# Kernel optimization log

Hardware: AMD Instinct MI355X
Metric: run time of the kernel (lower is better)

The kernel has to match this reference:

```python
import jax, jax.numpy as jnp
import numpy as np

N, D, F, H, L = 500000, 2, 128, 128, 8
OMEGA_0 = 30.0


def setup_inputs() -> dict:
    key = jax.random.key(0)
    ks = jax.random.split(key, 13)
    two_pi = 2.0 * np.pi
    w = 0.05  # weight init scale
    return {
        "S": jax.random.uniform(ks[0], (N, 1), jnp.float32),
        "t": jax.random.uniform(ks[1], (N, 1), jnp.float32),
        "B": jax.random.normal(ks[2], (D, F), jnp.float32) * two_pi,
        "in_w": jax.random.normal(ks[3], (2 * F, H), jnp.float32) * w,
        "in_b": jax.random.normal(ks[4], (H,), jnp.float32) * w,
        "blk_w1": jax.random.normal(ks[5], (L, H, H), jnp.float32) * w,
        "blk_b1": jax.random.normal(ks[6], (L, H), jnp.float32) * w,
        "blk_w2": jax.random.normal(ks[7], (L, H, H), jnp.float32) * w,
        "blk_b2": jax.random.normal(ks[8], (L, H), jnp.float32) * w,
        "skip_w": jax.random.normal(ks[9], ((L + 1) // 2, 2 * F, H), jnp.float32) * w,
        "skip_b": jax.random.normal(ks[10], ((L + 1) // 2, H), jnp.float32) * w,
        "out_w": jax.random.normal(ks[11], (H, 1), jnp.float32) * w,
        "out_b": jax.random.normal(ks[12], (1,), jnp.float32) * w,
    }


def reference(S, t, B, in_w, in_b, blk_w1, blk_b1, blk_w2, blk_b2,
              skip_w, skip_b, out_w, out_b):
    # Fourier feature mapping: [N,2] -> [N,2F]
    inputs = jnp.concatenate([S, t], axis=1)
    proj = inputs @ B                       # [N, F]
    ff = jnp.concatenate([jnp.sin(proj), jnp.cos(proj)], axis=-1)  # [N, 2F]
    # SIREN input layer
    x = jnp.sin(OMEGA_0 * (ff @ in_w + in_b))  # [N, H]
    n_blocks = blk_w1.shape[0]
    for i in range(n_blocks):  # small fixed layer loop
        h = jnp.tanh(x @ blk_w1[i] + blk_b1[i]) @ blk_w2[i] + blk_b2[i]
        x = x + h  # residual
        if i % 2 == 0:  # periodic skip from Fourier features
            x = x + ff @ skip_w[i // 2] + skip_b[i // 2]
    return x @ out_w + out_b  # [N, 1]
```

## Files before the change

kernel.cpp:

```cpp
#include <hip/hip_runtime.h>
#include <cstdint>
#include <cstddef>

#define NPTS 500000

using f16   = _Float16;
using f16x8 = __attribute__((ext_vector_type(8))) _Float16;
using f32x4 = __attribute__((ext_vector_type(4))) float;
using f32x16= __attribute__((ext_vector_type(16))) float;

#define WS_INW   0u
#define WS_SKIP  65536u
#define WS_W1    327680u
#define WS_W2    589824u
#define WS_BIAS  851968u
#define WS_BC    863232u
#define WS_OB    864256u
#define WS_TOTAL 864272u

__device__ __host__ __forceinline__ int phi(int m) {
  return (m & ~12) | ((m & 4) << 1) | ((m & 8) >> 1);
}

extern "C" __global__ void pinn_prep(const float* __restrict__ in_w,
                                     const float* __restrict__ w1,
                                     const float* __restrict__ w2,
                                     const float* __restrict__ skw,
                                     const float* __restrict__ inb,
                                     const float* __restrict__ b1,
                                     const float* __restrict__ b2,
                                     const float* __restrict__ skb,
                                     const float* __restrict__ ow,
                                     const float* __restrict__ ob,
                                     const float* __restrict__ Bg,
                                     char* __restrict__ ws) {
  int idx = (int)blockIdx.x * 256 + (int)threadIdx.x;
  if (idx < 32768) {
    int H = idx >> 14, r = idx & 16383, m = r >> 7, c = r & 127;
    int gl = c >> 5, sc = (c >> 4) & 1, lo = c & 15;
    int k = sc * 128 + (H * 4 + gl) * 16 + lo;
    uint32_t off = (uint32_t)(m * 256 + c * 2) ^ (uint32_t)((m & 15) << 4);
    *(f16*)(ws + WS_INW + (uint32_t)H * 32768u + off) = (f16)in_w[k * 128 + phi(m)];
  } else if (idx < 163840) {
    int r0 = idx - 32768;
    int j4 = r0 >> 15, rr = r0 & 32767;
    int H = rr >> 14, r = rr & 16383, m = r >> 7, c = r & 127;
    int gl = c >> 5, sc = (c >> 4) & 1, lo = c & 15;
    int k = sc * 128 + (H * 4 + gl) * 16 + lo;
    uint32_t off = (uint32_t)(m * 256 + c * 2) ^ (uint32_t)((m & 15) << 4);
    *(f16*)(ws + WS_SKIP + (uint32_t)j4 * 65536u + (uint32_t)H * 32768u + off) =
        (f16)skw[(j4 * 256 + k) * 128 + phi(m)];
  } else if (idx < 294912) {
    int r0 = idx - 163840;
    int i = r0 >> 14, r = r0 & 16383, m = r >> 7, k = r & 127;
    uint32_t off = (uint32_t)(m * 256 + k * 2) ^ (uint32_t)((m & 15) << 4);
    *(f16*)(ws + WS_W1 + (uint32_t)i * 32768u + off) = (f16)w1[(i * 128 + k) * 128 + phi(m)];
  } else if (idx < 425984) {
    int r0 = idx - 294912;
    int i = r0 >> 14, r = r0 & 16383, m = r >> 7, k = r & 127;
    uint32_t off = (uint32_t)(m * 256 + k * 2) ^ (uint32_t)((m & 15) << 4);
    *(f16*)(ws + WS_W2 + (uint32_t)i * 32768u + off) = (f16)w2[(i * 128 + k) * 128 + phi(m)];
  } else if (idx < 428800) {
    int r = idx - 425984;
    int M = r >> 7, pos = r & 127;
    int pp = phi(pos);
    float v;
    if (M == 0)        v = inb[pp];
    else if (M <= 16)  { int t = M - 1; int i = t >> 1; v = (t & 1) ? b2[i * 128 + pp] : b1[i * 128 + pp]; }
    else if (M <= 20)  v = skb[(M - 17) * 128 + pp];
    else               v = ow[pp];
    *(float*)(ws + WS_BIAS + (uint32_t)r * 4u) = v;
  } else if (idx < 429056) {
    int r = idx - 428800;
    int slot = r >> 4, e2 = r & 15;
    int kq = slot >> 1, hb = slot & 1;
    int row = e2 >> 3, e = e2 & 7;
    int j = kq * 16 + hb * 8 + e;
    *(float*)(ws + WS_BC + (uint32_t)r * 4u) = Bg[row * 128 + j] * 0.15915494309189535f;
  } else if (idx == 429056) {
    *(float*)(ws + WS_OB) = ob[0];
    *(float*)(ws + WS_OB + 4) = 0.f; *(float*)(ws + WS_OB + 8) = 0.f; *(float*)(ws + WS_OB + 12) = 0.f;
  }
}

__device__ __forceinline__ float ftanh(float x) {
  float e = __builtin_amdgcn_exp2f(x * 2.8853901817f);
  return 1.0f - 2.0f * __builtin_amdgcn_rcpf(e + 1.0f);
}
__device__ __forceinline__ float fsin_rev(float rev) {
  return __builtin_amdgcn_sinf(__builtin_amdgcn_fractf(rev));
}

__device__ __forceinline__ void gll16(const char* g, char* l) {
  __builtin_amdgcn_global_load_lds((const __attribute__((address_space(1))) void*)g,
                                   (__attribute__((address_space(3))) void*)l, 16, 0, 0);
}
__device__ __forceinline__ void stage32(const char* g, char* l, int wv, int ln64) {
  const char* gs = g + wv * 4096 + ln64 * 16;
  char* ls = l + wv * 4096;
  #pragma unroll
  for (int it = 0; it < 4; ++it) gll16(gs + it * 1024, ls + it * 1024);
}

#define MFMA_(a,b,c)  __builtin_amdgcn_mfma_f32_32x32x16_f16(a,b,c,0,0,0)

#define LDW(BASE, MT, KB) (*(const f16x8*)((BASE) + \
  ((((uint32_t)(MT)*32u + lnr)*256u + (uint32_t)(KB)*32u + hi16v) ^ SW16)))

#define BINIT(acc, Mi, MT) { const float* _bp = biasL + ((Mi)*128 + (MT)*32 + hi4); \
  f32x4 _q0 = *(const f32x4*)_bp;        f32x4 _q1 = *(const f32x4*)(_bp+8); \
  f32x4 _q2 = *(const f32x4*)(_bp+16);   f32x4 _q3 = *(const f32x4*)(_bp+24); \
  acc[0]=_q0[0]; acc[1]=_q0[1]; acc[2]=_q0[2]; acc[3]=_q0[3]; \
  acc[4]=_q1[0]; acc[5]=_q1[1]; acc[6]=_q1[2]; acc[7]=_q1[3]; \
  acc[8]=_q2[0]; acc[9]=_q2[1]; acc[10]=_q2[2]; acc[11]=_q2[3]; \
  acc[12]=_q3[0]; acc[13]=_q3[1]; acc[14]=_q3[2]; acc[15]=_q3[3]; }

#define UNPADD(acc, F0, F1) { \
  acc[0]+=(float)F0[0]; acc[1]+=(float)F0[1]; acc[2]+=(float)F0[2]; acc[3]+=(float)F0[3]; \
  acc[4]+=(float)F0[4]; acc[5]+=(float)F0[5]; acc[6]+=(float)F0[6]; acc[7]+=(float)F0[7]; \
  acc[8]+=(float)F1[0]; acc[9]+=(float)F1[1]; acc[10]+=(float)F1[2]; acc[11]+=(float)F1[3]; \
  acc[12]+=(float)F1[4]; acc[13]+=(float)F1[5]; acc[14]+=(float)F1[6]; acc[15]+=(float)F1[7]; }

#define FPACK(F0, F1, acc) { f16x8 _g0, _g1; \
  _g0[0]=(f16)acc[0]; _g0[1]=(f16)acc[1]; _g0[2]=(f16)acc[2]; _g0[3]=(f16)acc[3]; \
  _g0[4]=(f16)acc[4]; _g0[5]=(f16)acc[5]; _g0[6]=(f16)acc[6]; _g0[7]=(f16)acc[7]; \
  _g1[0]=(f16)acc[8]; _g1[1]=(f16)acc[9]; _g1[2]=(f16)acc[10]; _g1[3]=(f16)acc[11]; \
  _g1[4]=(f16)acc[12]; _g1[5]=(f16)acc[13]; _g1[6]=(f16)acc[14]; _g1[7]=(f16)acc[15]; \
  F0=_g0; F1=_g1; }

#define TPACK(F0, F1, acc) { f16x8 _g0, _g1; \
  _g0[0]=(f16)ftanh(acc[0]); _g0[1]=(f16)ftanh(acc[1]); _g0[2]=(f16)ftanh(acc[2]); _g0[3]=(f16)ftanh(acc[3]); \
  _g0[4]=(f16)ftanh(acc[4]); _g0[5]=(f16)ftanh(acc[5]); _g0[6]=(f16)ftanh(acc[6]); _g0[7]=(f16)ftanh(acc[7]); \
  _g1[0]=(f16)ftanh(acc[8]); _g1[1]=(f16)ftanh(acc[9]); _g1[2]=(f16)ftanh(acc[10]); _g1[3]=(f16)ftanh(acc[11]); \
  _g1[4]=(f16)ftanh(acc[12]); _g1[5]=(f16)ftanh(acc[13]); _g1[6]=(f16)ftanh(acc[14]); _g1[7]=(f16)ftanh(acc[15]); \
  F0=_g0; F1=_g1; }

#define OM2PI 4.7746482927f
#define SINPACK(F0, F1, acc) { f16x8 _g0, _g1; \
  _g0[0]=(f16)fsin_rev(acc[0]*OM2PI); _g0[1]=(f16)fsin_rev(acc[1]*OM2PI); \
  _g0[2]=(f16)fsin_rev(acc[2]*OM2PI); _g0[3]=(f16)fsin_rev(acc[3]*OM2PI); \
  _g0[4]=(f16)fsin_rev(acc[4]*OM2PI); _g0[5]=(f16)fsin_rev(acc[5]*OM2PI); \
  _g0[6]=(f16)fsin_rev(acc[6]*OM2PI); _g0[7]=(f16)fsin_rev(acc[7]*OM2PI); \
  _g1[0]=(f16)fsin_rev(acc[8]*OM2PI); _g1[1]=(f16)fsin_rev(acc[9]*OM2PI); \
  _g1[2]=(f16)fsin_rev(acc[10]*OM2PI); _g1[3]=(f16)fsin_rev(acc[11]*OM2PI); \
  _g1[4]=(f16)fsin_rev(acc[12]*OM2PI); _g1[5]=(f16)fsin_rev(acc[13]*OM2PI); \
  _g1[6]=(f16)fsin_rev(acc[14]*OM2PI); _g1[7]=(f16)fsin_rev(acc[15]*OM2PI); \
  F0=_g0; F1=_g1; }

#define FFE(ei, CA, CB) { \
  float _r = __builtin_amdgcn_fractf(sv*(CA) + tv*(CB)); \
  _s[ei] = (f16)__builtin_amdgcn_sinf(_r); _c[ei] = (f16)__builtin_amdgcn_cosf(_r); }
#define FF2(G, FS, FC) { const float* _cp = BcL + ((G)*2 + hi)*16; \
  f32x4 _a0 = *(const f32x4*)_cp, _a1 = *(const f32x4*)(_cp+4); \
  f32x4 _b0 = *(const f32x4*)(_cp+8), _b1 = *(const f32x4*)(_cp+12); \
  f16x8 _s, _c; \
  FFE(0,_a0[0],_b0[0]) FFE(1,_a0[1],_b0[1]) FFE(2,_a0[2],_b0[2]) FFE(3,_a0[3],_b0[3]) \
  FFE(4,_a1[0],_b1[0]) FFE(5,_a1[1],_b1[1]) FFE(6,_a1[2],_b1[2]) FFE(7,_a1[3],_b1[3]) \
  FS = _s; FC = _c; }

#define FFG(G, SLOT) { f16x8 _fs,_fc; FF2(G,_fs,_fc) \
  { f16x8 _w=LDW(SLOT,0,((G)&3)*2);   a0=MFMA_(_w,_fs,a0); } \
  { f16x8 _w=LDW(SLOT,0,((G)&3)*2+1); a0=MFMA_(_w,_fc,a0); } \
  { f16x8 _w=LDW(SLOT,1,((G)&3)*2);   a1=MFMA_(_w,_fs,a1); } \
  { f16x8 _w=LDW(SLOT,1,((G)&3)*2+1); a1=MFMA_(_w,_fc,a1); } \
  { f16x8 _w=LDW(SLOT,2,((G)&3)*2);   a2=MFMA_(_w,_fs,a2); } \
  { f16x8 _w=LDW(SLOT,2,((G)&3)*2+1); a2=MFMA_(_w,_fc,a2); } \
  { f16x8 _w=LDW(SLOT,3,((G)&3)*2);   a3=MFMA_(_w,_fs,a3); } \
  { f16x8 _w=LDW(SLOT,3,((G)&3)*2+1); a3=MFMA_(_w,_fc,a3); } }

#define W1K(kb) { f16x8 _a = LDW(sA_, MTv, kb); acc = MFMA_(_a, x##kb, acc); }
#define W1TILE(MT, U0, U1) { const uint32_t MTv = (MT); \
  f32x16 acc; BINIT(acc, Mw1, MT) \
  W1K(0) W1K(1) W1K(2) W1K(3) W1K(4) W1K(5) W1K(6) W1K(7) \
  TPACK(U0, U1, acc) }

#define W2K(kb) { f16x8 _a = LDW(sB_, MTv, kb); acc = MFMA_(_a, u##kb, acc); }
#define W2TILE(MT, X0, X1) { const uint32_t MTv = (MT); \
  f32x16 acc; BINIT(acc, Mw2, MT) \
  W2K(0) W2K(1) W2K(2) W2K(3) W2K(4) W2K(5) W2K(6) W2K(7) \
  f16x8 _t0,_t1; FPACK(_t0,_t1,acc) X0 = X0 + _t0; X1 = X1 + _t1; }

#define OWDOT(P, F0, F1, bp) P += (float)F0[0]*bp[0] + (float)F0[1]*bp[1] + (float)F0[2]*bp[2] + (float)F0[3]*bp[3] \
  + (float)F0[4]*bp[8]  + (float)F0[5]*bp[9]  + (float)F0[6]*bp[10] + (float)F0[7]*bp[11] \
  + (float)F1[0]*bp[16] + (float)F1[1]*bp[17] + (float)F1[2]*bp[18] + (float)F1[3]*bp[19] \
  + (float)F1[4]*bp[24] + (float)F1[5]*bp[25] + (float)F1[6]*bp[26] + (float)F1[7]*bp[27];

extern "C" __global__ void __launch_bounds__(512, 2)
pinn_main(const float* __restrict__ Sg, const float* __restrict__ Tg,
          const char* __restrict__ ws, float* __restrict__ outg)
{
  extern __shared__ char smem[];
  char* sAw = smem;          const char* sA_ = sAw;
  char* sBw = smem + 32768;  const char* sB_ = sBw;
  const float* biasL = (const float*)(smem + 65536);
  const float* BcL   = biasL + 2816;

  const int tid  = (int)threadIdx.x;
  const int lane = tid & 63;
  const int wave = tid >> 6;
  const int hi   = lane >> 5;
  const uint32_t lnr   = (uint32_t)(lane & 31);
  const uint32_t hi16v = (uint32_t)hi * 16u;
  const uint32_t SW16  = (lnr & 15u) << 4;
  const int hi4  = hi * 4;

  const int pt = (int)blockIdx.x * 256 + wave * 32 + (int)lnr;
  const int q  = pt < NPTS ? pt : NPTS - 1;
  const float sv = Sg[q], tv = Tg[q];

  #pragma unroll 1
  for (int o = tid * 16; o < 12304; o += 8192)
    *(f32x4*)(smem + 65536 + o) = *(const f32x4*)(ws + WS_BIAS + o);
  stage32(ws + WS_INW,          sAw, wave, lane);
  stage32(ws + WS_INW + 32768u, sBw, wave, lane);
  __syncthreads();

  f16x8 x0,x1,x2,x3,x4,x5,x6,x7;
  f16x8 u0,u1,u2,u3,u4,u5,u6,u7;

  {
    f32x16 a0,a1,a2,a3;
    BINIT(a0,0,0) BINIT(a1,0,1) BINIT(a2,0,2) BINIT(a3,0,3)
    FFG(0, sA_) FFG(1, sA_) FFG(2, sA_) FFG(3, sA_)
    __syncthreads();
    stage32(ws + WS_W1, sAw, wave, lane);
    FFG(4, sB_) FFG(5, sB_) FFG(6, sB_) FFG(7, sB_)
    __syncthreads();
    stage32(ws + WS_W2, sBw, wave, lane);
    SINPACK(x0,x1,a0) SINPACK(x2,x3,a1) SINPACK(x4,x5,a2) SINPACK(x6,x7,a3)
  }

  #pragma unroll 1
  for (int i = 0; i < 8; ++i) {
    const int Mw1 = 1 + 2 * i, Mw2 = 2 + 2 * i;

    __syncthreads();
    W1TILE(0, u0,u1) W1TILE(1, u2,u3) W1TILE(2, u4,u5) W1TILE(3, u6,u7)
    __syncthreads();
    if ((i & 1) == 0) stage32(ws + WS_SKIP + (uint32_t)(i >> 1) * 65536u, sAw, wave, lane);
    else if (i < 7)   stage32(ws + WS_W1 + (uint32_t)(i + 1) * 32768u, sAw, wave, lane);

    W2TILE(0, x0,x1) W2TILE(1, x2,x3) W2TILE(2, x4,x5) W2TILE(3, x6,x7)
    __syncthreads();
    if ((i & 1) == 0) stage32(ws + WS_SKIP + (uint32_t)(i >> 1) * 65536u + 32768u, sBw, wave, lane);
    else if (i < 7)   stage32(ws + WS_W2 + (uint32_t)(i + 1) * 32768u, sBw, wave, lane);

    if ((i & 1) == 0) {
      const int Msk = 17 + (i >> 1);
      __syncthreads();
      f32x16 a0,a1,a2,a3;
      BINIT(a0,Msk,0) BINIT(a1,Msk,1) BINIT(a2,Msk,2) BINIT(a3,Msk,3)
      UNPADD(a0, x0,x1) UNPADD(a1, x2,x3) UNPADD(a2, x4,x5) UNPADD(a3, x6,x7)
      FFG(0, sA_) FFG(1, sA_) FFG(2, sA_) FFG(3, sA_)
      __syncthreads();
      stage32(ws + WS_W1 + (uint32_t)(i + 1) * 32768u, sAw, wave, lane);
      FFG(4, sB_) FFG(5, sB_) FFG(6, sB_) FFG(7, sB_)
      __syncthreads();
      stage32(ws + WS_W2 + (uint32_t)(i + 1) * 32768u, sBw, wave, lane);
      FPACK(x0,x1,a0) FPACK(x2,x3,a1) FPACK(x4,x5,a2) FPACK(x6,x7,a3)
    }
  }

  float p = 0.0f;
  { const float* bp = biasL + 21 * 128 + 0 * 32 + hi4; OWDOT(p, x0, x1, bp) }
  { const float* bp = biasL + 21 * 128 + 1 * 32 + hi4; OWDOT(p, x2, x3, bp) }
  { const float* bp = biasL + 21 * 128 + 2 * 32 + hi4; OWDOT(p, x4, x5, bp) }
  { const float* bp = biasL + 21 * 128 + 3 * 32 + hi4; OWDOT(p, x6, x7, bp) }
  p += __shfl_xor(p, 32);
  if (hi == 0 && pt < NPTS) outg[pt] = p + biasL[3072];
}

extern "C" void kernel_launch(void* const* d_in, const int* in_sizes, int n_in,
                              void* d_out, int out_size, void* d_ws, size_t ws_size,
                              hipStream_t stream) {
  (void)in_sizes; (void)n_in; (void)out_size;
  const float* S   = (const float*)d_in[0];
  const float* T   = (const float*)d_in[1];
  const float* B   = (const float*)d_in[2];
  const float* inw = (const float*)d_in[3];
  const float* inb = (const float*)d_in[4];
  const float* w1  = (const float*)d_in[5];
  const float* b1  = (const float*)d_in[6];
  const float* w2  = (const float*)d_in[7];
  const float* b2  = (const float*)d_in[8];
  const float* sw  = (const float*)d_in[9];
  const float* sb  = (const float*)d_in[10];
  const float* ow  = (const float*)d_in[11];
  const float* ob  = (const float*)d_in[12];
  char* ws   = (char*)d_ws;
  float* out = (float*)d_out;
  if (ws_size < (size_t)WS_TOTAL) return;

  pinn_prep<<<1677, 256, 0, stream>>>(inw, w1, w2, sw, inb, b1, b2, sb, ow, ob, B, ws);

  const int smem_bytes = 77840;
  hipFuncSetAttribute(reinterpret_cast<const void*>(pinn_main),
                      hipFuncAttributeMaxDynamicSharedMemorySize, smem_bytes);
  const int grid = (NPTS + 255) / 256;
  pinn_main<<<grid, 512, smem_bytes, stream>>>(S, T, ws, out);
}
```

Measured before the change: 533.2 us.

## Halve block size and use a single LDS weight slot with fp16 biases

Blocks shrink from 512 threads (256 points) to 256 threads (128 points), and LDS drops from two 32KB weight slots to one, with biases stored as fp16, cutting shared memory from about 78KB to about 39KB. The aim is to fit more blocks per CU (launch bounds 256,4) so more waves are resident to hide latency. The trade-off is that weight staging can no longer be double-buffered: each stage is followed by a barrier before use, so global-to-LDS loads are exposed and there are more barriers. Each block also now stages the full weight set for half as many points. Biases lose precision by being rounded to fp16.

```diff
diff --git a/kernel.cpp b/kernel.cpp
--- a/kernel.cpp
+++ b/kernel.cpp
@@ -5,6 +5,7 @@
 #define NPTS 500000
 
 using f16   = _Float16;
+using f16x4 = __attribute__((ext_vector_type(4))) _Float16;
 using f16x8 = __attribute__((ext_vector_type(8))) _Float16;
 using f32x4 = __attribute__((ext_vector_type(4))) float;
 using f32x16= __attribute__((ext_vector_type(16))) float;
@@ -69,7 +70,7 @@
     else if (M <= 16)  { int t = M - 1; int i = t >> 1; v = (t & 1) ? b2[i * 128 + pp] : b1[i * 128 + pp]; }
     else if (M <= 20)  v = skb[(M - 17) * 128 + pp];
     else               v = ow[pp];
-    *(float*)(ws + WS_BIAS + (uint32_t)r * 4u) = v;
+    *(f16*)(ws + WS_BIAS + (uint32_t)r * 2u) = (f16)v;
   } else if (idx < 429056) {
     int r = idx - 428800;
     int slot = r >> 4, e2 = r & 15;
@@ -96,10 +97,10 @@
                                    (__attribute__((address_space(3))) void*)l, 16, 0, 0);
 }
 __device__ __forceinline__ void stage32(const char* g, char* l, int wv, int ln64) {
-  const char* gs = g + wv * 4096 + ln64 * 16;
-  char* ls = l + wv * 4096;
+  const char* gs = g + wv * 8192 + ln64 * 16;
+  char* ls = l + wv * 8192;
   #pragma unroll
-  for (int it = 0; it < 4; ++it) gll16(gs + it * 1024, ls + it * 1024);
+  for (int it = 0; it < 8; ++it) gll16(gs + it * 1024, ls + it * 1024);
 }
 
 #define MFMA_(a,b,c)  __builtin_amdgcn_mfma_f32_32x32x16_f16(a,b,c,0,0,0)
@@ -107,13 +108,13 @@
 #define LDW(BASE, MT, KB) (*(const f16x8*)((BASE) + \
   ((((uint32_t)(MT)*32u + lnr)*256u + (uint32_t)(KB)*32u + hi16v) ^ SW16)))
 
-#define BINIT(acc, Mi, MT) { const float* _bp = biasL + ((Mi)*128 + (MT)*32 + hi4); \
-  f32x4 _q0 = *(const f32x4*)_bp;        f32x4 _q1 = *(const f32x4*)(_bp+8); \
-  f32x4 _q2 = *(const f32x4*)(_bp+16);   f32x4 _q3 = *(const f32x4*)(_bp+24); \
-  acc[0]=_q0[0]; acc[1]=_q0[1]; acc[2]=_q0[2]; acc[3]=_q0[3]; \
-  acc[4]=_q1[0]; acc[5]=_q1[1]; acc[6]=_q1[2]; acc[7]=_q1[3]; \
-  acc[8]=_q2[0]; acc[9]=_q2[1]; acc[10]=_q2[2]; acc[11]=_q2[3]; \
-  acc[12]=_q3[0]; acc[13]=_q3[1]; acc[14]=_q3[2]; acc[15]=_q3[3]; }
+#define BINIT(acc, Mi, MT) { const f16* _bp = biasH + ((Mi)*128 + (MT)*32 + hi4); \
+  f16x4 _q0 = *(const f16x4*)_bp;        f16x4 _q1 = *(const f16x4*)(_bp+8); \
+  f16x4 _q2 = *(const f16x4*)(_bp+16);   f16x4 _q3 = *(const f16x4*)(_bp+24); \
+  acc[0]=(float)_q0[0]; acc[1]=(float)_q0[1]; acc[2]=(float)_q0[2]; acc[3]=(float)_q0[3]; \
+  acc[4]=(float)_q1[0]; acc[5]=(float)_q1[1]; acc[6]=(float)_q1[2]; acc[7]=(float)_q1[3]; \
+  acc[8]=(float)_q2[0]; acc[9]=(float)_q2[1]; acc[10]=(float)_q2[2]; acc[11]=(float)_q2[3]; \
+  acc[12]=(float)_q3[0]; acc[13]=(float)_q3[1]; acc[14]=(float)_q3[2]; acc[15]=(float)_q3[3]; }
 
 #define UNPADD(acc, F0, F1) { \
   acc[0]+=(float)F0[0]; acc[1]+=(float)F0[1]; acc[2]+=(float)F0[2]; acc[3]+=(float)F0[3]; \
@@ -158,42 +159,45 @@
   FFE(4,_a1[0],_b1[0]) FFE(5,_a1[1],_b1[1]) FFE(6,_a1[2],_b1[2]) FFE(7,_a1[3],_b1[3]) \
   FS = _s; FC = _c; }
 
-#define FFG(G, SLOT) { f16x8 _fs,_fc; FF2(G,_fs,_fc) \
-  { f16x8 _w=LDW(SLOT,0,((G)&3)*2);   a0=MFMA_(_w,_fs,a0); } \
-  { f16x8 _w=LDW(SLOT,0,((G)&3)*2+1); a0=MFMA_(_w,_fc,a0); } \
-  { f16x8 _w=LDW(SLOT,1,((G)&3)*2);   a1=MFMA_(_w,_fs,a1); } \
-  { f16x8 _w=LDW(SLOT,1,((G)&3)*2+1); a1=MFMA_(_w,_fc,a1); } \
-  { f16x8 _w=LDW(SLOT,2,((G)&3)*2);   a2=MFMA_(_w,_fs,a2); } \
-  { f16x8 _w=LDW(SLOT,2,((G)&3)*2+1); a2=MFMA_(_w,_fc,a2); } \
-  { f16x8 _w=LDW(SLOT,3,((G)&3)*2);   a3=MFMA_(_w,_fs,a3); } \
-  { f16x8 _w=LDW(SLOT,3,((G)&3)*2+1); a3=MFMA_(_w,_fc,a3); } }
-
-#define W1K(kb) { f16x8 _a = LDW(sA_, MTv, kb); acc = MFMA_(_a, x##kb, acc); }
+#define FFG(G) { f16x8 _fs,_fc; FF2(G,_fs,_fc) \
+  { f16x8 _w=LDW(sS_,0,((G)&3)*2);   a0=MFMA_(_w,_fs,a0); } \
+  { f16x8 _w=LDW(sS_,0,((G)&3)*2+1); a0=MFMA_(_w,_fc,a0); } \
+  { f16x8 _w=LDW(sS_,1,((G)&3)*2);   a1=MFMA_(_w,_fs,a1); } \
+  { f16x8 _w=LDW(sS_,1,((G)&3)*2+1); a1=MFMA_(_w,_fc,a1); } \
+  { f16x8 _w=LDW(sS_,2,((G)&3)*2);   a2=MFMA_(_w,_fs,a2); } \
+  { f16x8 _w=LDW(sS_,2,((G)&3)*2+1); a2=MFMA_(_w,_fc,a2); } \
+  { f16x8 _w=LDW(sS_,3,((G)&3)*2);   a3=MFMA_(_w,_fs,a3); } \
+  { f16x8 _w=LDW(sS_,3,((G)&3)*2+1); a3=MFMA_(_w,_fc,a3); } }
+
+#define W1K(kb) { f16x8 _a = LDW(sS_, MTv, kb); acc = MFMA_(_a, x##kb, acc); }
 #define W1TILE(MT, U0, U1) { const uint32_t MTv = (MT); \
   f32x16 acc; BINIT(acc, Mw1, MT) \
   W1K(0) W1K(1) W1K(2) W1K(3) W1K(4) W1K(5) W1K(6) W1K(7) \
   TPACK(U0, U1, acc) }
 
-#define W2K(kb) { f16x8 _a = LDW(sB_, MTv, kb); acc = MFMA_(_a, u##kb, acc); }
+#define W2K(kb) { f16x8 _a = LDW(sS_, MTv, kb); acc = MFMA_(_a, u##kb, acc); }
 #define W2TILE(MT, X0, X1) { const uint32_t MTv = (MT); \
   f32x16 acc; BINIT(acc, Mw2, MT) \
   W2K(0) W2K(1) W2K(2) W2K(3) W2K(4) W2K(5) W2K(6) W2K(7) \
   f16x8 _t0,_t1; FPACK(_t0,_t1,acc) X0 = X0 + _t0; X1 = X1 + _t1; }
 
-#define OWDOT(P, F0, F1, bp) P += (float)F0[0]*bp[0] + (float)F0[1]*bp[1] + (float)F0[2]*bp[2] + (float)F0[3]*bp[3] \
-  + (float)F0[4]*bp[8]  + (float)F0[5]*bp[9]  + (float)F0[6]*bp[10] + (float)F0[7]*bp[11] \
-  + (float)F1[0]*bp[16] + (float)F1[1]*bp[17] + (float)F1[2]*bp[18] + (float)F1[3]*bp[19] \
-  + (float)F1[4]*bp[24] + (float)F1[5]*bp[25] + (float)F1[6]*bp[26] + (float)F1[7]*bp[27];
-
-extern "C" __global__ void __launch_bounds__(512, 2)
+#define OWDOT(P, F0, F1, bp) P += (float)F0[0]*(float)bp[0] + (float)F0[1]*(float)bp[1] \
+  + (float)F0[2]*(float)bp[2]  + (float)F0[3]*(float)bp[3] \
+  + (float)F0[4]*(float)bp[8]  + (float)F0[5]*(float)bp[9] \
+  + (float)F0[6]*(float)bp[10] + (float)F0[7]*(float)bp[11] \
+  + (float)F1[0]*(float)bp[16] + (float)F1[1]*(float)bp[17] \
+  + (float)F1[2]*(float)bp[18] + (float)F1[3]*(float)bp[19] \
+  + (float)F1[4]*(float)bp[24] + (float)F1[5]*(float)bp[25] \
+  + (float)F1[6]*(float)bp[26] + (float)F1[7]*(float)bp[27];
+
+extern "C" __global__ void __launch_bounds__(256, 4)
 pinn_main(const float* __restrict__ Sg, const float* __restrict__ Tg,
           const char* __restrict__ ws, float* __restrict__ outg)
 {
   extern __shared__ char smem[];
-  char* sAw = smem;          const char* sA_ = sAw;
-  char* sBw = smem + 32768;  const char* sB_ = sBw;
-  const float* biasL = (const float*)(smem + 65536);
-  const float* BcL   = biasL + 2816;
+  char* sSw = smem;          const char* sS_ = sSw;
+  const f16*   biasH = (const f16*)(smem + 32768);
+  const float* BcL   = (const float*)(smem + 38416);
 
   const int tid  = (int)threadIdx.x;
   const int lane = tid & 63;
@@ -204,15 +208,16 @@
   const uint32_t SW16  = (lnr & 15u) << 4;
   const int hi4  = hi * 4;
 
-  const int pt = (int)blockIdx.x * 256 + wave * 32 + (int)lnr;
+  const int pt = (int)blockIdx.x * 128 + wave * 32 + (int)lnr;
   const int q  = pt < NPTS ? pt : NPTS - 1;
   const float sv = Sg[q], tv = Tg[q];
 
   #pragma unroll 1
-  for (int o = tid * 16; o < 12304; o += 8192)
-    *(f32x4*)(smem + 65536 + o) = *(const f32x4*)(ws + WS_BIAS + o);
-  stage32(ws + WS_INW,          sAw, wave, lane);
-  stage32(ws + WS_INW + 32768u, sBw, wave, lane);
+  for (int o = tid * 16; o < 5648; o += 4096)
+    *(f32x4*)(smem + 32768 + o) = *(const f32x4*)(ws + WS_BIAS + o);
+  if (tid < 65)
+    *(f32x4*)(smem + 38416 + tid * 16) = *(const f32x4*)(ws + WS_BC + tid * 16);
+  stage32(ws + WS_INW, sSw, wave, lane);
   __syncthreads();
 
   f16x8 x0,x1,x2,x3,x4,x5,x6,x7;
@@ -221,14 +226,15 @@
   {
     f32x16 a0,a1,a2,a3;
     BINIT(a0,0,0) BINIT(a1,0,1) BINIT(a2,0,2) BINIT(a3,0,3)
-    FFG(0, sA_) FFG(1, sA_) FFG(2, sA_) FFG(3, sA_)
-    __syncthreads();
-    stage32(ws + WS_W1, sAw, wave, lane);
-    FFG(4, sB_) FFG(5, sB_) FFG(6, sB_) FFG(7, sB_)
-    __syncthreads();
-    stage32(ws + WS_W2, sBw, wave, lane);
+    FFG(0) FFG(1) FFG(2) FFG(3)
+    __syncthreads();
+    stage32(ws + WS_INW + 32768u, sSw, wave, lane);
+    __syncthreads();
+    FFG(4) FFG(5) FFG(6) FFG(7)
     SINPACK(x0,x1,a0) SINPACK(x2,x3,a1) SINPACK(x4,x5,a2) SINPACK(x6,x7,a3)
   }
+  __syncthreads();
+  stage32(ws + WS_W1, sSw, wave, lane);
 
   #pragma unroll 1
   for (int i = 0; i < 8; ++i) {
@@ -237,37 +243,39 @@
     __syncthreads();
     W1TILE(0, u0,u1) W1TILE(1, u2,u3) W1TILE(2, u4,u5) W1TILE(3, u6,u7)
     __syncthreads();
-    if ((i & 1) == 0) stage32(ws + WS_SKIP + (uint32_t)(i >> 1) * 65536u, sAw, wave, lane);
-    else if (i < 7)   stage32(ws + WS_W1 + (uint32_t)(i + 1) * 32768u, sAw, wave, lane);
-
+    stage32(ws + WS_W2 + (uint32_t)i * 32768u, sSw, wave, lane);
+    __syncthreads();
     W2TILE(0, x0,x1) W2TILE(1, x2,x3) W2TILE(2, x4,x5) W2TILE(3, x6,x7)
     __syncthreads();
-    if ((i & 1) == 0) stage32(ws + WS_SKIP + (uint32_t)(i >> 1) * 65536u + 32768u, sBw, wave, lane);
-    else if (i < 7)   stage32(ws + WS_W2 + (uint32_t)(i + 1) * 32768u, sBw, wave, lane);
 
     if ((i & 1) == 0) {
-      const int Msk = 17 + (i >> 1);
-      __syncthreads();
+      const int j = i >> 1;
+      const int Msk = 17 + j;
+      stage32(ws + WS_SKIP + (uint32_t)j * 65536u, sSw, wave, lane);
       f32x16 a0,a1,a2,a3;
       BINIT(a0,Msk,0) BINIT(a1,Msk,1) BINIT(a2,Msk,2) BINIT(a3,Msk,3)
       UNPADD(a0, x0,x1) UNPADD(a1, x2,x3) UNPADD(a2, x4,x5) UNPADD(a3, x6,x7)
-      FFG(0, sA_) FFG(1, sA_) FFG(2, sA_) FFG(3, sA_)
       __syncthreads();
-      stage32(ws + WS_W1 + (uint32_t)(i + 1) * 32768u, sAw, wave, lane);
-      FFG(4, sB_) FFG(5, sB_) FFG(6, sB_) FFG(7, sB_)
+      FFG(0) FFG(1) FFG(2) FFG(3)
       __syncthreads();
-      stage32(ws + WS_W2 + (uint32_t)(i + 1) * 32768u, sBw, wave, lane);
+      stage32(ws + WS_SKIP + (uint32_t)j * 65536u + 32768u, sSw, wave, lane);
+      __syncthreads();
+      FFG(4) FFG(5) FFG(6) FFG(7)
       FPACK(x0,x1,a0) FPACK(x2,x3,a1) FPACK(x4,x5,a2) FPACK(x6,x7,a3)
+      __syncthreads();
+      stage32(ws + WS_W1 + (uint32_t)(i + 1) * 32768u, sSw, wave, lane);
+    } else if (i < 7) {
+      stage32(ws + WS_W1 + (uint32_t)(i + 1) * 32768u, sSw, wave, lane);
     }
   }
 
   float p = 0.0f;
-  { const float* bp = biasL + 21 * 128 + 0 * 32 + hi4; OWDOT(p, x0, x1, bp) }
-  { const float* bp = biasL + 21 * 128 + 1 * 32 + hi4; OWDOT(p, x2, x3, bp) }
-  { const float* bp = biasL + 21 * 128 + 2 * 32 + hi4; OWDOT(p, x4, x5, bp) }
-  { const float* bp = biasL + 21 * 128 + 3 * 32 + hi4; OWDOT(p, x6, x7, bp) }
+  { const f16* bp = biasH + 21 * 128 + 0 * 32 + hi4; OWDOT(p, x0, x1, bp) }
+  { const f16* bp = biasH + 21 * 128 + 1 * 32 + hi4; OWDOT(p, x2, x3, bp) }
+  { const f16* bp = biasH + 21 * 128 + 2 * 32 + hi4; OWDOT(p, x4, x5, bp) }
+  { const f16* bp = biasH + 21 * 128 + 3 * 32 + hi4; OWDOT(p, x6, x7, bp) }
   p += __shfl_xor(p, 32);
-  if (hi == 0 && pt < NPTS) outg[pt] = p + biasL[3072];
+  if (hi == 0 && pt < NPTS) outg[pt] = p + BcL[256];
 }
 
 extern "C" void kernel_launch(void* const* d_in, const int* in_sizes, int n_in,
@@ -293,9 +301,9 @@
 
   pinn_prep<<<1677, 256, 0, stream>>>(inw, w1, w2, sw, inb, b1, b2, sb, ow, ob, B, ws);
 
-  const int smem_bytes = 77840;
+  const int smem_bytes = 39456;
   hipFuncSetAttribute(reinterpret_cast<const void*>(pinn_main),
                       hipFuncAttributeMaxDynamicSharedMemorySize, smem_bytes);
-  const int grid = (NPTS + 255) / 256;
-  pinn_main<<<grid, 512, smem_bytes, stream>>>(S, T, ws, out);
-}
+  const int grid = (NPTS + 127) / 128;
+  pinn_main<<<grid, 256, smem_bytes, stream>>>(S, T, ws, out);
+}
```

After: 700.9 us. 1.31x slower.
